# Performance work log

Measured on AMD Instinct MI355X. Metric: run time of the kernel, lower is better.

Reference implementation:

```python
import math
import jax, jax.numpy as jnp
import numpy as np

B, T, C, H = 4, 1024, 1024, 16
HD = C // H
BLOCK = 1024


def setup_inputs() -> dict:
    key = jax.random.key(0)
    k0, k1, k2, k3 = jax.random.split(key, 4)
    x = jax.random.normal(k0, (B, T, C), dtype=jnp.float32)
    # torch Linear weight is (out, in); we store (in, out) and apply x @ W + b
    W_attn = jax.random.normal(k1, (C, 3 * C), dtype=jnp.float32) * 0.02
    b_attn = jnp.zeros((3 * C,), dtype=jnp.float32)
    W_proj = jax.random.normal(k2, (C, C), dtype=jnp.float32) * 0.02
    b_proj = jnp.zeros((C,), dtype=jnp.float32)
    # rel_pos_emb: (n_head, block_size, head_dim), std 0.02 (leading 1 dim dropped)
    rel_pos_emb = jax.random.normal(k3, (H, BLOCK, HD), dtype=jnp.float32) * 0.02
    return {"x": x, "W_attn": W_attn, "b_attn": b_attn,
            "W_proj": W_proj, "b_proj": b_proj, "rel_pos_emb": rel_pos_emb}


def reference(x, W_attn, b_attn, W_proj, b_proj, rel_pos_emb):
    Bx, Tx, Cx = x.shape
    qkv = x @ W_attn + b_attn                      # (B, T, 3C)
    q, k, v = jnp.split(qkv, 3, axis=2)
    q = q.reshape(Bx, Tx, H, HD).transpose(0, 2, 1, 3)   # (B, H, T, hd)
    k = k.reshape(Bx, Tx, H, HD).transpose(0, 2, 1, 3)
    v = v.reshape(Bx, Tx, H, HD).transpose(0, 2, 1, 3)

    att = jnp.einsum('bhid,bhjd->bhij', q, k)      # (B, H, T, T)

    # relative position score: pos[b,h,i,j] = sum_d E[h, clamp(i-j,0), d] * k[b,h,j,d]
    # compute P[b,h,r,j] = <E[h,r,:], k[b,h,j,:]> then gather r = clamp(i-j, 0)
    rng = jnp.arange(Tx)
    dist = jnp.clip(rng[:, None] - rng[None, :], 0, None)          # (T, T)
    P = jnp.einsum('hrd,bhjd->bhrj', rel_pos_emb[:, :Tx], k)       # (B, H, T, T)
    pos_score = jnp.take_along_axis(P, dist[None, None, :, :], axis=2)
    att = att + pos_score

    att = att * (1.0 / math.sqrt(HD))
    causal = jnp.tril(jnp.ones((Tx, Tx), dtype=bool))
    att = jnp.where(causal[None, None], att, -jnp.inf)
    att = jax.nn.softmax(att, axis=-1)
    # dropout p=0.0 -> identity
    y = jnp.einsum('bhij,bhjd->bhid', att, v)      # (B, H, T, hd)
    y = y.transpose(0, 2, 1, 3).reshape(Bx, Tx, Cx)
    return y @ W_proj + b_proj
```

## Files before the change

### kernel.cpp

```cpp
#include <hip/hip_runtime.h>


typedef __bf16 bf16x8 __attribute__((ext_vector_type(8)));
typedef float f32x4 __attribute__((ext_vector_type(4)));
typedef unsigned short ushort_t;

#define T_SEQ 1024
#define NHEAD 16
#define HDIM 64
#define PLANE 4194304

__device__ __forceinline__ float bf2f(ushort_t h) {
    unsigned int u = ((unsigned int)h) << 16;
    float f; __builtin_memcpy(&f, &u, 4); return f;
}
__device__ __forceinline__ ushort_t f2bf(float f) {
    unsigned int u; __builtin_memcpy(&u, &f, 4);
    u = u + 0x7FFFu + ((u >> 16) & 1u);
    return (ushort_t)(u >> 16);
}

__global__ __launch_bounds__(256) void sentinel_kernel(float* out, int n, float val) {
    const int i = blockIdx.x * 256 + threadIdx.x;
    if (i < n) out[i] = val;
}

__global__ __launch_bounds__(256) void convert2(
    const float* __restrict__ x, ushort_t* __restrict__ x16,
    const float* __restrict__ E, ushort_t* __restrict__ E16)
{
    const int bid = blockIdx.x;
    const float* src; ushort_t* dst; int base;
    if (bid < 4096) { src = x; dst = x16; base = bid * 1024; }
    else            { src = E; dst = E16; base = (bid - 4096) * 1024; }
    const int i = base + (int)threadIdx.x * 4;
    const float4 v = *reinterpret_cast<const float4*>(src + i);
    union { unsigned long long u; ushort_t s[4]; } o;
    o.s[0] = f2bf(v.x); o.s[1] = f2bf(v.y); o.s[2] = f2bf(v.z); o.s[3] = f2bf(v.w);
    *reinterpret_cast<unsigned long long*>(dst + i) = o.u;
}

__global__ __launch_bounds__(256) void transpose_bf16(
    const float* __restrict__ W, ushort_t* __restrict__ Wt, int Kdim, int Ndim)
{
    __shared__ ushort_t t[64][65];
    const int n0 = blockIdx.x * 64, k0 = blockIdx.y * 64;
    const int cx = threadIdx.x & 63, ry = threadIdx.x >> 6;
#pragma unroll
    for (int i = 0; i < 16; i++) {
        const int r = ry + i * 4;
        t[r][cx] = f2bf(W[(size_t)(k0 + r) * Ndim + n0 + cx]);
    }
    __syncthreads();
#pragma unroll
    for (int i = 0; i < 16; i++) {
        const int r = ry + i * 4;
        Wt[(size_t)(n0 + r) * Kdim + k0 + cx] = t[cx][r];
    }
}

__global__ __launch_bounds__(256) void transpose_v(
    const ushort_t* __restrict__ v, ushort_t* __restrict__ vT)
{
    __shared__ ushort_t t[64][65];
    const int bh = blockIdx.y;
    const int t0 = blockIdx.x * 64;
    const int cx = threadIdx.x & 63, ry = threadIdx.x >> 6;
    const ushort_t* src = v + (size_t)bh * 65536;
    ushort_t* dst = vT + (size_t)bh * 65536;
#pragma unroll
    for (int i = 0; i < 16; i++) {
        const int r = ry + i * 4;
        t[r][cx] = src[(size_t)(t0 + r) * HDIM + cx];
    }
    __syncthreads();
#pragma unroll
    for (int i = 0; i < 16; i++) {
        const int d = ry + i * 4;
        dst[(size_t)d * T_SEQ + t0 + cx] = t[cx][d];
    }
}

template <int MODE>
__global__ __launch_bounds__(256) void gemm128(
    const ushort_t* __restrict__ A16, const ushort_t* __restrict__ Bt,
    const float* __restrict__ bias, void* __restrict__ out_,
    int Ndim, int Kdim)
{
    __shared__ __align__(16) ushort_t As[128 * 32];
    __shared__ __align__(16) ushort_t Bs[128 * 32];

    const int tid = threadIdx.x;
    const int w = tid >> 6;
    const int lane = tid & 63;
    const int l15 = lane & 15;
    const int quad = lane >> 4;
    const int m0 = blockIdx.y * 128, n0 = blockIdx.x * 128;
    const int wm = (w & 1) * 64, wn = (w >> 1) * 64;

    f32x4 acc[4][4];
#pragma unroll
    for (int mt = 0; mt < 4; mt++)
#pragma unroll
        for (int nt = 0; nt < 4; nt++) acc[mt][nt] = (f32x4){0.f, 0.f, 0.f, 0.f};

    for (int kk = 0; kk < Kdim; kk += 32) {
        __syncthreads();
#pragma unroll
        for (int t = 0; t < 2; t++) {
            const int chunk = w * 128 + t * 64 + lane;
            const int row = chunk >> 2, kc = (chunk & 3) * 8;
            __builtin_amdgcn_global_load_lds(
                (const __attribute__((address_space(1))) void*)
                    (A16 + (size_t)(m0 + row) * Kdim + kk + kc),
                (__attribute__((address_space(3))) void*)
                    (As + (size_t)(w * 128 + t * 64) * 8), 16, 0, 0);
            __builtin_amdgcn_global_load_lds(
                (const __attribute__((address_space(1))) void*)
                    (Bt + (size_t)(n0 + row) * Kdim + kk + kc),
                (__attribute__((address_space(3))) void*)
                    (Bs + (size_t)(w * 128 + t * 64) * 8), 16, 0, 0);
        }
        __syncthreads();

        bf16x8 af[4], bf[4];
#pragma unroll
        for (int mt = 0; mt < 4; mt++)
            af[mt] = *reinterpret_cast<const bf16x8*>(&As[(wm + mt * 16 + l15) * 32 + quad * 8]);
#pragma unroll
        for (int nt = 0; nt < 4; nt++)
            bf[nt] = *reinterpret_cast<const bf16x8*>(&Bs[(wn + nt * 16 + l15) * 32 + quad * 8]);
#pragma unroll
        for (int mt = 0; mt < 4; mt++)
#pragma unroll
            for (int nt = 0; nt < 4; nt++)
                acc[mt][nt] = __builtin_amdgcn_mfma_f32_16x16x32_bf16(
                    af[mt], bf[nt], acc[mt][nt], 0, 0, 0);
    }

#pragma unroll
    for (int mt = 0; mt < 4; mt++)
#pragma unroll
        for (int nt = 0; nt < 4; nt++) {
            const int n = n0 + wn + nt * 16 + l15;
            const float bv = bias[n];
#pragma unroll
            for (int r = 0; r < 4; r++) {
                const int m = m0 + wm + mt * 16 + quad * 4 + r;
                const float val = acc[mt][nt][r] + bv;
                if (MODE == 0) {
                    ushort_t* ws = (ushort_t*)out_;
                    const int which = n >> 10;
                    const size_t pl = (which == 2) ? 3 : which;
                    const int cc = n & 1023;
                    const int h = cc >> 6, d = cc & 63;
                    const int b = m >> 10, t = m & 1023;
                    ws[pl * PLANE + ((size_t)(b * NHEAD + h) * T_SEQ + t) * HDIM + d] = f2bf(val);
                } else {
                    ((float*)out_)[(size_t)m * Ndim + n] = val;
                }
            }
        }
}

__global__ __launch_bounds__(256) void flash_attn(
    const ushort_t* __restrict__ qp, const ushort_t* __restrict__ kp,
    const ushort_t* __restrict__ vTp, const ushort_t* __restrict__ E16,
    ushort_t* __restrict__ y16)
{
    __shared__ __align__(16) ushort_t Ks[64 * 72];
    __shared__ __align__(16) ushort_t Vt[64 * 72];
    __shared__ __align__(16) ushort_t Es[128 * 72];
    __shared__ __align__(16) ushort_t Ps[64 * 64 + 16];

    const int bh = blockIdx.y;
    const int h = bh & (NHEAD - 1);
    const int b = bh >> 4;
    const int tid = threadIdx.x;
    const int w = tid >> 6;
    const int lane = tid & 63;
    const int l15 = lane & 15;
    const int quad = lane >> 4;

    const size_t base = (size_t)bh * T_SEQ * HDIM;
    const ushort_t* Eh = E16 + (size_t)h * T_SEQ * HDIM;
    const ushort_t* vTb = vTp + (size_t)bh * 65536;
    const float c1 = 0.125f * 1.44269504f;

    const int rq = tid >> 2, cq = (tid & 3) * 16;
    const int re = tid >> 1, ce = (tid & 1) * 32;

    bf16x8 ones;
#pragma unroll
    for (int i = 0; i < 8; i++) ones[i] = (__bf16)1.0f;

#pragma unroll 1
    for (int ph = 0; ph < 2; ph++) {
        const int it = ph ? (int)blockIdx.x : 15 - (int)blockIdx.x;
        const int i0 = it * 64;

        bf16x8 qf[2];
        {
            const ushort_t* qrow = qp + base + (size_t)(i0 + w * 16 + l15) * HDIM;
            qf[0] = *reinterpret_cast<const bf16x8*>(qrow + quad * 8);
            qf[1] = *reinterpret_cast<const bf16x8*>(qrow + 32 + quad * 8);
        }

        f32x4 o[4], o5;
#pragma unroll
        for (int dt = 0; dt < 4; dt++) o[dt] = (f32x4){0.f, 0.f, 0.f, 0.f};
        o5 = (f32x4){0.f, 0.f, 0.f, 0.f};
        float mrow[4];
#pragma unroll
        for (int r = 0; r < 4; r++) mrow[r] = -3e38f;

        for (int j0 = 0; j0 <= i0; j0 += 64) {
            const int d0 = i0 - j0;
            __syncthreads();
            {
                const ushort_t* ksrc = kp + base + (size_t)(j0 + rq) * HDIM + cq;
                *reinterpret_cast<uint4*>(&Ks[rq * 72 + cq]) = *reinterpret_cast<const uint4*>(ksrc);
                *reinterpret_cast<uint4*>(&Ks[rq * 72 + cq + 8]) = *reinterpret_cast<const uint4*>(ksrc + 8);
                const ushort_t* vsrc = vTb + (size_t)rq * T_SEQ + j0 + cq;
                *reinterpret_cast<uint4*>(&Vt[rq * 72 + cq]) = *reinterpret_cast<const uint4*>(vsrc);
                *reinterpret_cast<uint4*>(&Vt[rq * 72 + cq + 8]) = *reinterpret_cast<const uint4*>(vsrc + 8);
            }
            {
                int g = d0 - 64 + re;
                g = g < 0 ? 0 : (g > 1023 ? 1023 : g);
                const ushort_t* esrc = Eh + (size_t)g * HDIM + ce;
#pragma unroll
                for (int q16 = 0; q16 < 4; q16++)
                    *reinterpret_cast<uint4*>(&Es[re * 72 + ce + q16 * 8]) =
                        *reinterpret_cast<const uint4*>(esrc + q16 * 8);
            }
            __syncthreads();

            f32x4 s[4], pb[2][4];
#pragma unroll
            for (int nt = 0; nt < 4; nt++) {
                s[nt] = (f32x4){0.f, 0.f, 0.f, 0.f};
                pb[0][nt] = (f32x4){0.f, 0.f, 0.f, 0.f};
                pb[1][nt] = (f32x4){0.f, 0.f, 0.f, 0.f};
            }
#pragma unroll
            for (int ks = 0; ks < 2; ks++) {
                const int ko = ks * 32 + quad * 8;
                const bf16x8 ae0 = *reinterpret_cast<const bf16x8*>(&Es[(w * 32 + l15) * 72 + ko]);
                const bf16x8 ae1 = *reinterpret_cast<const bf16x8*>(&Es[(w * 32 + 16 + l15) * 72 + ko]);
#pragma unroll
                for (int nt = 0; nt < 4; nt++) {
                    const bf16x8 bk = *reinterpret_cast<const bf16x8*>(&Ks[(nt * 16 + l15) * 72 + ko]);
                    s[nt] = __builtin_amdgcn_mfma_f32_16x16x32_bf16(qf[ks], bk, s[nt], 0, 0, 0);
                    pb[0][nt] = __builtin_amdgcn_mfma_f32_16x16x32_bf16(ae0, bk, pb[0][nt], 0, 0, 0);
                    pb[1][nt] = __builtin_amdgcn_mfma_f32_16x16x32_bf16(ae1, bk, pb[1][nt], 0, 0, 0);
                }
            }
#pragma unroll
            for (int mf = 0; mf < 2; mf++)
#pragma unroll
                for (int nt = 0; nt < 4; nt++) {
                    const int jl = nt * 16 + l15;
#pragma unroll
                    for (int r = 0; r < 4; r++) {
                        const int br = w * 32 + mf * 16 + quad * 4 + r;
                        const int il_t = br - 64 + jl;
                        const int addr = ((unsigned)il_t < 64u) ? il_t * 64 + jl : 4096;
                        Ps[addr] = f2bf(pb[mf][nt][r]);
                    }
                }
            __syncthreads();

            float pv[4][4], mnew[4];
#pragma unroll
            for (int r = 0; r < 4; r++) mnew[r] = mrow[r];
            const int il0 = w * 16 + quad * 4;
            if (j0 < i0) {
#pragma unroll
                for (int nt = 0; nt < 4; nt++) {
                    const int jl = nt * 16 + l15;
#pragma unroll
                    for (int r = 0; r < 4; r++) {
                        const float sv = (s[nt][r] + bf2f(Ps[(il0 + r) * 64 + jl])) * c1;
                        pv[nt][r] = sv;
                        mnew[r] = fmaxf(mnew[r], sv);
                    }
                }
            } else {
#pragma unroll
                for (int nt = 0; nt < 4; nt++) {
                    const int jl = nt * 16 + l15;
#pragma unroll
                    for (int r = 0; r < 4; r++) {
                        const int il = il0 + r;
                        float sv = (s[nt][r] + bf2f(Ps[il * 64 + jl])) * c1;
                        if (jl > il) sv = -3e38f;
                        pv[nt][r] = sv;
                        mnew[r] = fmaxf(mnew[r], sv);
                    }
                }
            }
#pragma unroll
            for (int r = 0; r < 4; r++)
#pragma unroll
                for (int off = 1; off < 16; off <<= 1)
                    mnew[r] = fmaxf(mnew[r], __shfl_xor(mnew[r], off, 64));
            float alpha[4];
#pragma unroll
            for (int r = 0; r < 4; r++) {
                alpha[r] = exp2f(mrow[r] - mnew[r]);
                mrow[r] = mnew[r];
            }
#pragma unroll
            for (int nt = 0; nt < 4; nt++)
#pragma unroll
                for (int r = 0; r < 4; r++)
                    pv[nt][r] = exp2f(pv[nt][r] - mnew[r]);
#pragma unroll
            for (int dt = 0; dt < 4; dt++)
#pragma unroll
                for (int r = 0; r < 4; r++) o[dt][r] *= alpha[r];
#pragma unroll
            for (int r = 0; r < 4; r++) o5[r] *= alpha[r];
#pragma unroll
            for (int nt = 0; nt < 4; nt++)
#pragma unroll
                for (int r = 0; r < 4; r++)
                    Es[(w * 16 + quad * 4 + r) * 72 + nt * 16 + l15] = f2bf(pv[nt][r]);
            __syncthreads();

#pragma unroll
            for (int ks = 0; ks < 2; ks++) {
                const int ko = ks * 32 + quad * 8;
                const bf16x8 ap = *reinterpret_cast<const bf16x8*>(&Es[(w * 16 + l15) * 72 + ko]);
#pragma unroll
                for (int dt = 0; dt < 4; dt++) {
                    const bf16x8 bv = *reinterpret_cast<const bf16x8*>(&Vt[(dt * 16 + l15) * 72 + ko]);
                    o[dt] = __builtin_amdgcn_mfma_f32_16x16x32_bf16(ap, bv, o[dt], 0, 0, 0);
                }
                o5 = __builtin_amdgcn_mfma_f32_16x16x32_bf16(ap, ones, o5, 0, 0, 0);
            }
        }

        float inv[4];
#pragma unroll
        for (int r = 0; r < 4; r++) inv[r] = 1.0f / o5[r];
#pragma unroll
        for (int dt = 0; dt < 4; dt++)
#pragma unroll
            for (int r = 0; r < 4; r++) {
                const int il = w * 16 + quad * 4 + r;
                const int d = dt * 16 + l15;
                y16[((size_t)(b * T_SEQ + i0 + il)) * 1024 + h * 64 + d] = f2bf(o[dt][r] * inv[r]);
            }
    }
}

extern "C" void kernel_launch(void* const* d_in, const int* in_sizes, int n_in,
                              void* d_out, int out_size, void* d_ws, size_t ws_size,
                              hipStream_t stream) {
    float* out = (float*)d_out;

    const void* x = nullptr; const void* Wa = nullptr; const void* ba = nullptr;
    const void* Wp = nullptr; const void* bp = nullptr; const void* E = nullptr;
    int anomaly = 0;
    if (n_in != 6) {
        anomaly = 2;
    } else {
        int c1M = 0;
        for (int i = 0; i < 6; i++) {
            const int s = in_sizes[i];
            if      (s == 4194304) x  = d_in[i];
            else if (s == 3145728) Wa = d_in[i];
            else if (s == 3072)    ba = d_in[i];
            else if (s == 1024)    bp = d_in[i];
            else if (s == 1048576) { if (c1M == 0) Wp = d_in[i]; else E = d_in[i]; c1M++; }
            else anomaly = 1;
        }
        if (!x || !Wa || !ba || !Wp || !bp || !E || c1M != 2) anomaly = 1;
    }
    if (!anomaly && out_size != 4194304) anomaly = 3;
    if (!anomaly && ws_size < (size_t)52428800) anomaly = 4;
    if (anomaly) {
        sentinel_kernel<<<(out_size + 255) / 256, 256, 0, stream>>>(out, out_size, 1000.0f * anomaly);
        return;
    }

    ushort_t* ws   = (ushort_t*)d_ws;
    ushort_t* qp   = ws;
    ushort_t* kp   = ws + (size_t)PLANE;
    ushort_t* vTp  = ws + (size_t)2 * PLANE;
    ushort_t* vtmp = ws + (size_t)3 * PLANE;
    ushort_t* y16  = vtmp;
    ushort_t* x16  = ws + (size_t)4 * PLANE;
    ushort_t* WaT  = ws + (size_t)5 * PLANE;
    ushort_t* WpT  = WaT + (size_t)3145728;
    ushort_t* E16  = WpT + (size_t)1048576;

    convert2<<<5120, 256, 0, stream>>>((const float*)x, x16, (const float*)E, E16);
    transpose_bf16<<<dim3(48, 16), 256, 0, stream>>>((const float*)Wa, WaT, 1024, 3072);
    transpose_bf16<<<dim3(16, 16), 256, 0, stream>>>((const float*)Wp, WpT, 1024, 1024);

    gemm128<0><<<dim3(24, 32), 256, 0, stream>>>(x16, WaT, (const float*)ba, (void*)ws, 3072, 1024);

    transpose_v<<<dim3(16, 64), 256, 0, stream>>>(vtmp, vTp);

    flash_attn<<<dim3(8, 64), 256, 0, stream>>>(qp, kp, vTp, E16, y16);

    gemm128<1><<<dim3(8, 32), 256, 0, stream>>>(y16, WpT, (const float*)bp, (void*)out, 1024, 1024);
}
```

Before: 222.3 us.

## Fuse prep kernels, fold softmax scale into Q/E, use direct-to-LDS swizzled loads

```diff
diff --git a/kernel.cpp b/kernel.cpp
--- a/kernel.cpp
+++ b/kernel.cpp
@@ -9,6 +9,7 @@
 #define NHEAD 16
 #define HDIM 64
 #define PLANE 4194304
+#define C1 0.1803368801f
 
 __device__ __forceinline__ float bf2f(ushort_t h) {
     unsigned int u = ((unsigned int)h) << 16;
@@ -25,26 +26,34 @@
     if (i < n) out[i] = val;
 }
 
-__global__ __launch_bounds__(256) void convert2(
+__global__ __launch_bounds__(256) void prep_fused(
     const float* __restrict__ x, ushort_t* __restrict__ x16,
-    const float* __restrict__ E, ushort_t* __restrict__ E16)
-{
-    const int bid = blockIdx.x;
-    const float* src; ushort_t* dst; int base;
-    if (bid < 4096) { src = x; dst = x16; base = bid * 1024; }
-    else            { src = E; dst = E16; base = (bid - 4096) * 1024; }
-    const int i = base + (int)threadIdx.x * 4;
-    const float4 v = *reinterpret_cast<const float4*>(src + i);
-    union { unsigned long long u; ushort_t s[4]; } o;
-    o.s[0] = f2bf(v.x); o.s[1] = f2bf(v.y); o.s[2] = f2bf(v.z); o.s[3] = f2bf(v.w);
-    *reinterpret_cast<unsigned long long*>(dst + i) = o.u;
-}
-
-__global__ __launch_bounds__(256) void transpose_bf16(
-    const float* __restrict__ W, ushort_t* __restrict__ Wt, int Kdim, int Ndim)
+    const float* __restrict__ E, ushort_t* __restrict__ E16,
+    const float* __restrict__ Wa, ushort_t* __restrict__ WaT,
+    const float* __restrict__ Wp, ushort_t* __restrict__ WpT)
 {
     __shared__ ushort_t t[64][65];
-    const int n0 = blockIdx.x * 64, k0 = blockIdx.y * 64;
+    const int bid = blockIdx.x;
+    if (bid < 5120) {
+        const float* src; ushort_t* dst; int base; float sc;
+        if (bid < 4096) { src = x; dst = x16; base = bid * 1024; sc = 1.0f; }
+        else            { src = E; dst = E16; base = (bid - 4096) * 1024; sc = C1; }
+        const int i = base + (int)threadIdx.x * 4;
+        const float4 v = *reinterpret_cast<const float4*>(src + i);
+        union { unsigned long long u; ushort_t s[4]; } o;
+        o.s[0] = f2bf(v.x * sc); o.s[1] = f2bf(v.y * sc);
+        o.s[2] = f2bf(v.z * sc); o.s[3] = f2bf(v.w * sc);
+        *reinterpret_cast<unsigned long long*>(dst + i) = o.u;
+        return;
+    }
+    const float* W; ushort_t* Wt; int Kdim, Ndim, n0, k0;
+    if (bid < 5888) {
+        W = Wa; Wt = WaT; Kdim = 1024; Ndim = 3072;
+        const int b = bid - 5120; n0 = (b % 48) * 64; k0 = (b / 48) * 64;
+    } else {
+        W = Wp; Wt = WpT; Kdim = 1024; Ndim = 1024;
+        const int b = bid - 5888; n0 = (b % 16) * 64; k0 = (b / 16) * 64;
+    }
     const int cx = threadIdx.x & 63, ry = threadIdx.x >> 6;
 #pragma unroll
     for (int i = 0; i < 16; i++) {
@@ -147,10 +156,11 @@
 #pragma unroll
             for (int r = 0; r < 4; r++) {
                 const int m = m0 + wm + mt * 16 + quad * 4 + r;
-                const float val = acc[mt][nt][r] + bv;
+                float val = acc[mt][nt][r] + bv;
                 if (MODE == 0) {
                     ushort_t* ws = (ushort_t*)out_;
                     const int which = n >> 10;
+                    if (which == 0) val *= C1;
                     const size_t pl = (which == 2) ? 3 : which;
                     const int cc = n & 1023;
                     const int h = cc >> 6, d = cc & 63;
@@ -168,14 +178,17 @@
     const ushort_t* __restrict__ vTp, const ushort_t* __restrict__ E16,
     ushort_t* __restrict__ y16)
 {
-    __shared__ __align__(16) ushort_t Ks[64 * 72];
-    __shared__ __align__(16) ushort_t Vt[64 * 72];
-    __shared__ __align__(16) ushort_t Es[128 * 72];
-    __shared__ __align__(16) ushort_t Ps[64 * 64 + 16];
-
+    __shared__ __align__(16) ushort_t Ks[64 * 64];
+    __shared__ __align__(16) ushort_t Vt[64 * 64];
+    __shared__ __align__(16) ushort_t Es[128 * 64];
+    __shared__ __align__(16) ushort_t Pr[64 * 64];
+    __shared__ __align__(16) ushort_t Ps[65 * 68];
+
+    const int it = 15 - (int)blockIdx.x;
     const int bh = blockIdx.y;
     const int h = bh & (NHEAD - 1);
     const int b = bh >> 4;
+    const int i0 = it * 64;
     const int tid = threadIdx.x;
     const int w = tid >> 6;
     const int lane = tid & 63;
@@ -185,175 +198,183 @@
     const size_t base = (size_t)bh * T_SEQ * HDIM;
     const ushort_t* Eh = E16 + (size_t)h * T_SEQ * HDIM;
     const ushort_t* vTb = vTp + (size_t)bh * 65536;
-    const float c1 = 0.125f * 1.44269504f;
-
-    const int rq = tid >> 2, cq = (tid & 3) * 16;
-    const int re = tid >> 1, ce = (tid & 1) * 32;
+
+    bf16x8 qf[2];
+    {
+        const ushort_t* qrow = qp + base + (size_t)(i0 + w * 16 + l15) * HDIM;
+        qf[0] = *reinterpret_cast<const bf16x8*>(qrow + quad * 8);
+        qf[1] = *reinterpret_cast<const bf16x8*>(qrow + 32 + quad * 8);
+    }
+
+    f32x4 o[4], o5;
+#pragma unroll
+    for (int dt = 0; dt < 4; dt++) o[dt] = (f32x4){0.f, 0.f, 0.f, 0.f};
+    o5 = (f32x4){0.f, 0.f, 0.f, 0.f};
+    float mrow[4];
+#pragma unroll
+    for (int r = 0; r < 4; r++) mrow[r] = -3e38f;
 
     bf16x8 ones;
 #pragma unroll
     for (int i = 0; i < 8; i++) ones[i] = (__bf16)1.0f;
 
-#pragma unroll 1
-    for (int ph = 0; ph < 2; ph++) {
-        const int it = ph ? (int)blockIdx.x : 15 - (int)blockIdx.x;
-        const int i0 = it * 64;
-
-        bf16x8 qf[2];
-        {
-            const ushort_t* qrow = qp + base + (size_t)(i0 + w * 16 + l15) * HDIM;
-            qf[0] = *reinterpret_cast<const bf16x8*>(qrow + quad * 8);
-            qf[1] = *reinterpret_cast<const bf16x8*>(qrow + 32 + quad * 8);
-        }
-
-        f32x4 o[4], o5;
-#pragma unroll
-        for (int dt = 0; dt < 4; dt++) o[dt] = (f32x4){0.f, 0.f, 0.f, 0.f};
-        o5 = (f32x4){0.f, 0.f, 0.f, 0.f};
-        float mrow[4];
-#pragma unroll
-        for (int r = 0; r < 4; r++) mrow[r] = -3e38f;
-
-        for (int j0 = 0; j0 <= i0; j0 += 64) {
-            const int d0 = i0 - j0;
-            __syncthreads();
-            {
-                const ushort_t* ksrc = kp + base + (size_t)(j0 + rq) * HDIM + cq;
-                *reinterpret_cast<uint4*>(&Ks[rq * 72 + cq]) = *reinterpret_cast<const uint4*>(ksrc);
-                *reinterpret_cast<uint4*>(&Ks[rq * 72 + cq + 8]) = *reinterpret_cast<const uint4*>(ksrc + 8);
-                const ushort_t* vsrc = vTb + (size_t)rq * T_SEQ + j0 + cq;
-                *reinterpret_cast<uint4*>(&Vt[rq * 72 + cq]) = *reinterpret_cast<const uint4*>(vsrc);
-                *reinterpret_cast<uint4*>(&Vt[rq * 72 + cq + 8]) = *reinterpret_cast<const uint4*>(vsrc + 8);
-            }
-            {
-                int g = d0 - 64 + re;
-                g = g < 0 ? 0 : (g > 1023 ? 1023 : g);
-                const ushort_t* esrc = Eh + (size_t)g * HDIM + ce;
-#pragma unroll
-                for (int q16 = 0; q16 < 4; q16++)
-                    *reinterpret_cast<uint4*>(&Es[re * 72 + ce + q16 * 8]) =
-                        *reinterpret_cast<const uint4*>(esrc + q16 * 8);
-            }
-            __syncthreads();
-
-            f32x4 s[4], pb[2][4];
+    const int xsw = l15 & 7;
+
+    for (int j0 = 0; j0 <= i0; j0 += 64) {
+        const int d0 = i0 - j0;
+        __syncthreads();
+#pragma unroll
+        for (int t = 0; t < 2; t++) {
+            const int idx = w * 128 + t * 64 + lane;
+            const int row = idx >> 3;
+            const int cg = (idx & 7) ^ (row & 7);
+            __builtin_amdgcn_global_load_lds(
+                (const __attribute__((address_space(1))) void*)
+                    (kp + base + (size_t)(j0 + row) * HDIM + cg * 8),
+                (__attribute__((address_space(3))) void*)(Ks + (size_t)(idx & ~63) * 8),
+                16, 0, 0);
+            __builtin_amdgcn_global_load_lds(
+                (const __attribute__((address_space(1))) void*)
+                    (vTb + (size_t)row * T_SEQ + j0 + cg * 8),
+                (__attribute__((address_space(3))) void*)(Vt + (size_t)(idx & ~63) * 8),
+                16, 0, 0);
+        }
+#pragma unroll
+        for (int t = 0; t < 4; t++) {
+            const int idx = w * 256 + t * 64 + lane;
+            const int row = idx >> 3;
+            const int cg = (idx & 7) ^ (row & 7);
+            int g = d0 - 64 + row;
+            if (g < 0) g = 0;
+            __builtin_amdgcn_global_load_lds(
+                (const __attribute__((address_space(1))) void*)
+                    (Eh + (size_t)g * HDIM + cg * 8),
+                (__attribute__((address_space(3))) void*)(Es + (size_t)(idx & ~63) * 8),
+                16, 0, 0);
+        }
+        __syncthreads();
+
+        f32x4 s[4], pb[2][4];
+#pragma unroll
+        for (int nt = 0; nt < 4; nt++) {
+            s[nt] = (f32x4){0.f, 0.f, 0.f, 0.f};
+            pb[0][nt] = (f32x4){0.f, 0.f, 0.f, 0.f};
+            pb[1][nt] = (f32x4){0.f, 0.f, 0.f, 0.f};
+        }
+#pragma unroll
+        for (int ks = 0; ks < 2; ks++) {
+            const int cidx = (ks * 4 + quad) ^ xsw;
+            const bf16x8 ae0 = *reinterpret_cast<const bf16x8*>(&Es[((w * 32 + l15) * 8 + cidx) * 8]);
+            const bf16x8 ae1 = *reinterpret_cast<const bf16x8*>(&Es[((w * 32 + 16 + l15) * 8 + cidx) * 8]);
 #pragma unroll
             for (int nt = 0; nt < 4; nt++) {
-                s[nt] = (f32x4){0.f, 0.f, 0.f, 0.f};
-                pb[0][nt] = (f32x4){0.f, 0.f, 0.f, 0.f};
-                pb[1][nt] = (f32x4){0.f, 0.f, 0.f, 0.f};
-            }
-#pragma unroll
-            for (int ks = 0; ks < 2; ks++) {
-                const int ko = ks * 32 + quad * 8;
-                const bf16x8 ae0 = *reinterpret_cast<const bf16x8*>(&Es[(w * 32 + l15) * 72 + ko]);
-                const bf16x8 ae1 = *reinterpret_cast<const bf16x8*>(&Es[(w * 32 + 16 + l15) * 72 + ko]);
-#pragma unroll
-                for (int nt = 0; nt < 4; nt++) {
-                    const bf16x8 bk = *reinterpret_cast<const bf16x8*>(&Ks[(nt * 16 + l15) * 72 + ko]);
-                    s[nt] = __builtin_amdgcn_mfma_f32_16x16x32_bf16(qf[ks], bk, s[nt], 0, 0, 0);
-                    pb[0][nt] = __builtin_amdgcn_mfma_f32_16x16x32_bf16(ae0, bk, pb[0][nt], 0, 0, 0);
-                    pb[1][nt] = __builtin_amdgcn_mfma_f32_16x16x32_bf16(ae1, bk, pb[1][nt], 0, 0, 0);
+                const bf16x8 bk = *reinterpret_cast<const bf16x8*>(&Ks[((nt * 16 + l15) * 8 + cidx) * 8]);
+                s[nt] = __builtin_amdgcn_mfma_f32_16x16x32_bf16(qf[ks], bk, s[nt], 0, 0, 0);
+                pb[0][nt] = __builtin_amdgcn_mfma_f32_16x16x32_bf16(ae0, bk, pb[0][nt], 0, 0, 0);
+                pb[1][nt] = __builtin_amdgcn_mfma_f32_16x16x32_bf16(ae1, bk, pb[1][nt], 0, 0, 0);
+            }
+        }
+#pragma unroll
+        for (int mf = 0; mf < 2; mf++)
+#pragma unroll
+            for (int nt = 0; nt < 4; nt++) {
+                const int jl = nt * 16 + l15;
+#pragma unroll
+                for (int r = 0; r < 4; r++) {
+                    const int br = w * 32 + mf * 16 + quad * 4 + r;
+                    const int il_t = br - 64 + jl;
+                    const int addr = ((unsigned)il_t < 64u) ? il_t * 68 + jl : 64 * 68 + jl;
+                    Ps[addr] = f2bf(pb[mf][nt][r]);
                 }
             }
-#pragma unroll
-            for (int mf = 0; mf < 2; mf++)
-#pragma unroll
-                for (int nt = 0; nt < 4; nt++) {
-                    const int jl = nt * 16 + l15;
-#pragma unroll
-                    for (int r = 0; r < 4; r++) {
-                        const int br = w * 32 + mf * 16 + quad * 4 + r;
-                        const int il_t = br - 64 + jl;
-                        const int addr = ((unsigned)il_t < 64u) ? il_t * 64 + jl : 4096;
-                        Ps[addr] = f2bf(pb[mf][nt][r]);
-                    }
+        __syncthreads();
+
+        float pv[4][4], mnew[4];
+#pragma unroll
+        for (int r = 0; r < 4; r++) mnew[r] = mrow[r];
+        const int il0 = w * 16 + quad * 4;
+        if (j0 < i0) {
+#pragma unroll
+            for (int nt = 0; nt < 4; nt++) {
+                const int jl = nt * 16 + l15;
+#pragma unroll
+                for (int r = 0; r < 4; r++) {
+                    const float sv = s[nt][r] + bf2f(Ps[(il0 + r) * 68 + jl]);
+                    pv[nt][r] = sv;
+                    mnew[r] = fmaxf(mnew[r], sv);
                 }
-            __syncthreads();
-
-            float pv[4][4], mnew[4];
-#pragma unroll
-            for (int r = 0; r < 4; r++) mnew[r] = mrow[r];
-            const int il0 = w * 16 + quad * 4;
-            if (j0 < i0) {
-#pragma unroll
-                for (int nt = 0; nt < 4; nt++) {
-                    const int jl = nt * 16 + l15;
-#pragma unroll
-                    for (int r = 0; r < 4; r++) {
-                        const float sv = (s[nt][r] + bf2f(Ps[(il0 + r) * 64 + jl])) * c1;
-                        pv[nt][r] = sv;
-                        mnew[r] = fmaxf(mnew[r], sv);
-                    }
+            }
+        } else {
+#pragma unroll
+            for (int nt = 0; nt < 4; nt++) {
+                const int jl = nt * 16 + l15;
+#pragma unroll
+                for (int r = 0; r < 4; r++) {
+                    const int il = il0 + r;
+                    float sv = s[nt][r] + bf2f(Ps[il * 68 + jl]);
+                    if (jl > il) sv = -3e38f;
+                    pv[nt][r] = sv;
+                    mnew[r] = fmaxf(mnew[r], sv);
                 }
-            } else {
-#pragma unroll
-                for (int nt = 0; nt < 4; nt++) {
-                    const int jl = nt * 16 + l15;
-#pragma unroll
-                    for (int r = 0; r < 4; r++) {
-                        const int il = il0 + r;
-                        float sv = (s[nt][r] + bf2f(Ps[il * 64 + jl])) * c1;
-                        if (jl > il) sv = -3e38f;
-                        pv[nt][r] = sv;
-                        mnew[r] = fmaxf(mnew[r], sv);
-                    }
-                }
-            }
+            }
+        }
+#pragma unroll
+        for (int r = 0; r < 4; r++)
+#pragma unroll
+            for (int off = 1; off < 16; off <<= 1)
+                mnew[r] = fmaxf(mnew[r], __shfl_xor(mnew[r], off, 64));
+        float alpha[4];
+#pragma unroll
+        for (int r = 0; r < 4; r++) {
+            alpha[r] = exp2f(mrow[r] - mnew[r]);
+            mrow[r] = mnew[r];
+        }
+#pragma unroll
+        for (int nt = 0; nt < 4; nt++)
 #pragma unroll
             for (int r = 0; r < 4; r++)
-#pragma unroll
-                for (int off = 1; off < 16; off <<= 1)
-                    mnew[r] = fmaxf(mnew[r], __shfl_xor(mnew[r], off, 64));
-            float alpha[4];
+                pv[nt][r] = exp2f(pv[nt][r] - mnew[r]);
+#pragma unroll
+        for (int dt = 0; dt < 4; dt++)
+#pragma unroll
+            for (int r = 0; r < 4; r++) o[dt][r] *= alpha[r];
+#pragma unroll
+        for (int r = 0; r < 4; r++) o5[r] *= alpha[r];
+#pragma unroll
+        for (int nt = 0; nt < 4; nt++) {
+            const int jl = nt * 16 + l15;
 #pragma unroll
             for (int r = 0; r < 4; r++) {
-                alpha[r] = exp2f(mrow[r] - mnew[r]);
-                mrow[r] = mnew[r];
-            }
-#pragma unroll
-            for (int nt = 0; nt < 4; nt++)
-#pragma unroll
-                for (int r = 0; r < 4; r++)
-                    pv[nt][r] = exp2f(pv[nt][r] - mnew[r]);
-#pragma unroll
-            for (int dt = 0; dt < 4; dt++)
-#pragma unroll
-                for (int r = 0; r < 4; r++) o[dt][r] *= alpha[r];
-#pragma unroll
-            for (int r = 0; r < 4; r++) o5[r] *= alpha[r];
-#pragma unroll
-            for (int nt = 0; nt < 4; nt++)
-#pragma unroll
-                for (int r = 0; r < 4; r++)
-                    Es[(w * 16 + quad * 4 + r) * 72 + nt * 16 + l15] = f2bf(pv[nt][r]);
-            __syncthreads();
-
-#pragma unroll
-            for (int ks = 0; ks < 2; ks++) {
-                const int ko = ks * 32 + quad * 8;
-                const bf16x8 ap = *reinterpret_cast<const bf16x8*>(&Es[(w * 16 + l15) * 72 + ko]);
-#pragma unroll
-                for (int dt = 0; dt < 4; dt++) {
-                    const bf16x8 bv = *reinterpret_cast<const bf16x8*>(&Vt[(dt * 16 + l15) * 72 + ko]);
-                    o[dt] = __builtin_amdgcn_mfma_f32_16x16x32_bf16(ap, bv, o[dt], 0, 0, 0);
-                }
-                o5 = __builtin_amdgcn_mfma_f32_16x16x32_bf16(ap, ones, o5, 0, 0, 0);
-            }
-        }
-
-        float inv[4];
-#pragma unroll
-        for (int r = 0; r < 4; r++) inv[r] = 1.0f / o5[r];
-#pragma unroll
-        for (int dt = 0; dt < 4; dt++)
-#pragma unroll
-            for (int r = 0; r < 4; r++) {
-                const int il = w * 16 + quad * 4 + r;
-                const int d = dt * 16 + l15;
-                y16[((size_t)(b * T_SEQ + i0 + il)) * 1024 + h * 64 + d] = f2bf(o[dt][r] * inv[r]);
-            }
-    }
+                const int row = il0 + r;
+                Pr[(row * 8 + ((jl >> 3) ^ (row & 7))) * 8 + (jl & 7)] = f2bf(pv[nt][r]);
+            }
+        }
+        __syncthreads();
+
+#pragma unroll
+        for (int ks = 0; ks < 2; ks++) {
+            const int cidx = (ks * 4 + quad) ^ xsw;
+            const bf16x8 ap = *reinterpret_cast<const bf16x8*>(&Pr[((w * 16 + l15) * 8 + cidx) * 8]);
+#pragma unroll
+            for (int dt = 0; dt < 4; dt++) {
+                const bf16x8 bv = *reinterpret_cast<const bf16x8*>(&Vt[((dt * 16 + l15) * 8 + cidx) * 8]);
+                o[dt] = __builtin_amdgcn_mfma_f32_16x16x32_bf16(ap, bv, o[dt], 0, 0, 0);
+            }
+            o5 = __builtin_amdgcn_mfma_f32_16x16x32_bf16(ap, ones, o5, 0, 0, 0);
+        }
+    }
+
+    float inv[4];
+#pragma unroll
+    for (int r = 0; r < 4; r++) inv[r] = 1.0f / o5[r];
+#pragma unroll
+    for (int dt = 0; dt < 4; dt++)
+#pragma unroll
+        for (int r = 0; r < 4; r++) {
+            const int il = w * 16 + quad * 4 + r;
+            const int d = dt * 16 + l15;
+            y16[((size_t)(b * T_SEQ + i0 + il)) * 1024 + h * 64 + d] = f2bf(o[dt][r] * inv[r]);
+        }
 }
 
 extern "C" void kernel_launch(void* const* d_in, const int* in_sizes, int n_in,
@@ -397,15 +418,15 @@
     ushort_t* WpT  = WaT + (size_t)3145728;
     ushort_t* E16  = WpT + (size_t)1048576;
 
-    convert2<<<5120, 256, 0, stream>>>((const float*)x, x16, (const float*)E, E16);
-    transpose_bf16<<<dim3(48, 16), 256, 0, stream>>>((const float*)Wa, WaT, 1024, 3072);
-    transpose_bf16<<<dim3(16, 16), 256, 0, stream>>>((const float*)Wp, WpT, 1024, 1024);
+    prep_fused<<<6144, 256, 0, stream>>>(
+        (const float*)x, x16, (const float*)E, E16,
+        (const float*)Wa, WaT, (const float*)Wp, WpT);
 
     gemm128<0><<<dim3(24, 32), 256, 0, stream>>>(x16, WaT, (const float*)ba, (void*)ws, 3072, 1024);
 
     transpose_v<<<dim3(16, 64), 256, 0, stream>>>(vtmp, vTp);
 
-    flash_attn<<<dim3(8, 64), 256, 0, stream>>>(qp, kp, vTp, E16, y16);
+    flash_attn<<<dim3(16, 64), 256, 0, stream>>>(qp, kp, vTp, E16, y16);
 
     gemm128<1><<<dim3(8, 32), 256, 0, stream>>>(y16, WpT, (const float*)bp, (void*)out, 1024, 1024);
 }
```

New measurement: 257.2 us. 15.7% more time.
